# Performance work log

Hardware: AMD Instinct MI355X
Metric: run time of the kernel (lower is better)

## Reference

```python
import jax, jax.numpy as jnp
import numpy as np

N = 100000
E = 1600000
IN_DIM, HID, OUT = 128, 64, 64


def _gat(x, src, dst, W, a_src, a_dst, b, n):
    h = x @ W                                   # [N, F]
    a_s = (h * a_src).sum(-1)                   # [N]
    a_d = (h * a_dst).sum(-1)
    e = jax.nn.leaky_relu(a_s[src] + a_d[dst], negative_slope=0.2)  # [E]
    m = jax.ops.segment_max(e, dst, num_segments=n)
    ex = jnp.exp(e - m[dst])
    denom = jax.ops.segment_sum(ex, dst, num_segments=n)
    coef = ex / jnp.maximum(denom[dst], 1e-16)
    out = jax.ops.segment_sum(h[src] * coef[:, None], dst, num_segments=n)
    return out + b


def _gcn(x, src, dst, W, b, n):
    deg = jax.ops.segment_sum(jnp.ones_like(src, dtype=x.dtype), dst, num_segments=n)
    dinv = jnp.where(deg > 0, deg ** -0.5, 0.0)
    norm = dinv[src] * dinv[dst]                # [E]
    h = x @ W
    out = jax.ops.segment_sum(h[src] * norm[:, None], dst, num_segments=n)
    return out + b


def setup_inputs() -> dict:
    key = jax.random.key(0)
    ks = jax.random.split(key, 24)
    g = lambda k, shp, fan: jax.random.normal(k, shp, dtype=jnp.float32) * (1.0 / np.sqrt(fan))
    inp = {}
    inp['features'] = jax.random.normal(ks[0], (N, IN_DIM), dtype=jnp.float32)
    inp['edge_index'] = jax.random.randint(ks[1], (2, E), 0, N, dtype=jnp.int64)
    inp['node_mask'] = jax.random.randint(ks[2], (N,), 0, 2, dtype=jnp.int32)
    # GAT layer 1 (in->hid) and 2 (hid->out)
    inp['W_gat1'] = g(ks[3], (IN_DIM, HID), IN_DIM)
    inp['a_src1'] = g(ks[4], (HID,), HID)
    inp['a_dst1'] = g(ks[5], (HID,), HID)
    inp['b_gat1'] = jnp.zeros((HID,), jnp.float32)
    inp['W_gat2'] = g(ks[6], (HID, OUT), HID)
    inp['a_src2'] = g(ks[7], (OUT,), OUT)
    inp['a_dst2'] = g(ks[8], (OUT,), OUT)
    inp['b_gat2'] = jnp.zeros((OUT,), jnp.float32)
    # GCN layers
    inp['W_gcn1'] = g(ks[9], (IN_DIM, HID), IN_DIM)
    inp['b_gcn1'] = jnp.zeros((HID,), jnp.float32)
    inp['W_gcn2'] = g(ks[10], (HID, OUT), HID)
    inp['b_gcn2'] = jnp.zeros((OUT,), jnp.float32)
    # Decoder fc: 2*OUT -> IN_DIM
    inp['W_dec'] = g(ks[11], (2 * OUT, IN_DIM), 2 * OUT)
    inp['b_dec'] = jnp.zeros((IN_DIM,), jnp.float32)
    # Discriminator
    inp['W_d1'] = g(ks[12], (2 * OUT, 64), 2 * OUT)
    inp['b_d1'] = jnp.zeros((64,), jnp.float32)
    inp['W_d2'] = g(ks[13], (64, 32), 64)
    inp['b_d2'] = jnp.zeros((32,), jnp.float32)
    inp['W_d3'] = g(ks[14], (32, 1), 32)
    inp['b_d3'] = jnp.zeros((1,), jnp.float32)
    return inp


def reference(features, edge_index, node_mask,
              W_gat1, a_src1, a_dst1, b_gat1,
              W_gat2, a_src2, a_dst2, b_gat2,
              W_gcn1, b_gcn1, W_gcn2, b_gcn2,
              W_dec, b_dec,
              W_d1, b_d1, W_d2, b_d2, W_d3, b_d3):
    n = features.shape[0]
    src, dst = edge_index[0], edge_index[1]
    # node masking (eval-deterministic stand-in for mask_by_nodes_)
    x = jnp.where((node_mask == 1)[:, None], 0.0, features)
    # GAT branch (dropout is identity in eval mode)
    h_gat = jax.nn.elu(_gat(x, src, dst, W_gat1, a_src1, a_dst1, b_gat1, n))
    h_gat = _gat(h_gat, src, dst, W_gat2, a_src2, a_dst2, b_gat2, n)
    # GCN branch
    h_gcn = jax.nn.relu(_gcn(x, src, dst, W_gcn1, b_gcn1, n))
    h_gcn = _gcn(h_gcn, src, dst, W_gcn2, b_gcn2, n)
    encoded = jnp.concatenate([h_gat, h_gcn], axis=1)  # [N, 2*OUT]
    recon = jax.nn.relu(encoded @ W_dec + b_dec)        # Decoder (dropout off)
    d = jax.nn.relu(encoded @ W_d1 + b_d1)
    d = jax.nn.sigmoid(d @ W_d2 + b_d2)
    disc = d @ W_d3 + b_d3                              # [N, 1]
    return recon, encoded, disc
```

## Files before the change

kernel.cpp:

```cpp
#include <hip/hip_runtime.h>
#include <math.h>


#define INF_F __int_as_float(0x7f800000)
#define NSHARD 8

typedef __attribute__((ext_vector_type(8))) short bh8;
typedef __attribute__((ext_vector_type(4))) float f32x4;

__device__ __forceinline__ long edge_at(const void* p, int is64, long i) {
    if (is64) return (long)((const long long*)p)[i];
    return (long)((const int*)p)[i];
}

__device__ __forceinline__ unsigned short f2bf(float f) {
    unsigned u = __float_as_uint(f);
    return (unsigned short)((u + 0x7FFFu + ((u >> 16) & 1u)) >> 16);
}
__device__ __forceinline__ float bflo(unsigned p) { return __uint_as_float(p << 16); }
__device__ __forceinline__ float bfhi(unsigned p) { return __uint_as_float(p & 0xFFFF0000u); }
__device__ __forceinline__ unsigned pk2bf(float a, float b) {
    return (unsigned)f2bf(a) | ((unsigned)f2bf(b) << 16);
}

__global__ void k_detect(const int* ew, long words, int* flag) {
    long t = (long)blockIdx.x * blockDim.x + threadIdx.x;
    long stride = words / 8192; if (stride < 1) stride = 1;
    long w = 2 * (t * stride) + 1;
    if (t < 4096 && w < words) {
        if (ew[w] != 0) atomicOr(flag, 1);
    }
}

__global__ void k_deg(const void* edges, long E, const int* flag, int* deg) {
    long e = (long)blockIdx.x * blockDim.x + threadIdx.x;
    if (e >= E) return;
    int is64 = (*flag == 0);
    int d = (int)edge_at(edges, is64, E + e);
    atomicAdd(&deg[d], 1);
}

__global__ void k_scanA(const int* deg, int N, int* offs, int* blockSums) {
    __shared__ int s[256];
    int t = threadIdx.x;
    int i = blockIdx.x * 256 + t;
    int v = (i < N) ? deg[i] : 0;
    s[t] = v;
    for (int off = 1; off < 256; off <<= 1) {
        __syncthreads();
        int u = (t >= off) ? s[t - off] : 0;
        __syncthreads();
        s[t] += u;
    }
    __syncthreads();
    if (i < N) offs[i] = s[t] - v;
    if (t == 255) blockSums[blockIdx.x] = s[255];
}

__global__ void k_scanB(const int* blockSums, int nb, int* blockOff) {
    __shared__ int s[1024];
    int t = threadIdx.x;
    int v = (t < nb) ? blockSums[t] : 0;
    s[t] = v;
    for (int off = 1; off < 1024; off <<= 1) {
        __syncthreads();
        int u = (t >= off) ? s[t - off] : 0;
        __syncthreads();
        s[t] += u;
    }
    __syncthreads();
    if (t < nb) blockOff[t] = s[t] - v;
}

__global__ void k_scanC(int* offs, const int* blockOff, const int* deg,
                        float* dinv, int N, long E) {
    int i = blockIdx.x * 256 + threadIdx.x;
    if (i < N) {
        offs[i] += blockOff[i >> 8];
        int dg = deg[i];
        dinv[i] = dg > 0 ? rsqrtf((float)dg) : 0.0f;
    }
    if (i == 0) offs[N] = (int)E;
}

__global__ void k_fill(const void* edges, long E, const int* flag,
                       const int* offs, int* cursor, int* csr_src, int npp) {
    int bid = blockIdx.x;
    int shard = bid & (NSHARD - 1);
    long e = (long)(bid >> 3) * blockDim.x + threadIdx.x;
    if (e >= E) return;
    int is64 = (*flag == 0);
    int d = (int)edge_at(edges, is64, E + e);
    if (d / npp != shard) return;
    int s = (int)edge_at(edges, is64, e);
    int pos = offs[d] + atomicAdd(&cursor[d], 1);
    csr_src[pos] = s << 8;
}

__global__ __launch_bounds__(512) void k_dense1(
    const float* __restrict__ x, const int* __restrict__ mask,
    const float* __restrict__ Wa, const float* __restrict__ Wg,
    const float* __restrict__ aSrc, const float* __restrict__ aDst,
    const float* __restrict__ dinv,
    unsigned short* __restrict__ h16,
    float* __restrict__ a_s, float* __restrict__ a_d, int N)
{
    __shared__ float sW[8192 + 16 + 8192];
    int t = threadIdx.x;
    for (int i = t; i < 2048; i += 512) {
        ((float4*)sW)[i] = ((const float4*)Wa)[i];
        ((float4*)(sW + 8208))[i] = ((const float4*)Wg)[i];
    }
    __syncthreads();
    int base = blockIdx.x * 64;
    int tx = t & 31, ny = t >> 5;
    bool gat = tx < 16;
    int jc = (tx & 15) * 4;
    const float* Wp = gat ? sW : (sW + 8208);
    int gn0 = base + ny * 4;
    const float4* xp[4]; float mz[4];
#pragma unroll
    for (int n = 0; n < 4; ++n) {
        int gn = gn0 + n;
        int cl = (gn < N) ? gn : 0;
        xp[n] = (const float4*)(x + (long)cl * 128);
        mz[n] = (gn < N && mask[cl] != 1) ? 1.f : 0.f;
    }
    float acc[4][4];
#pragma unroll
    for (int n = 0; n < 4; ++n) { acc[n][0] = acc[n][1] = acc[n][2] = acc[n][3] = 0.f; }
#pragma unroll 2
    for (int k0 = 0; k0 < 128; k0 += 4) {
        float4 w[4];
#pragma unroll
        for (int kk = 0; kk < 4; ++kk) w[kk] = *(const float4*)&Wp[(k0 + kk) * 64 + jc];
        float4 xr[4];
#pragma unroll
        for (int n = 0; n < 4; ++n) xr[n] = xp[n][k0 >> 2];
#pragma unroll
        for (int kk = 0; kk < 4; ++kk) {
#pragma unroll
            for (int n = 0; n < 4; ++n) {
                float xv = (&xr[n].x)[kk];
                acc[n][0] = fmaf(xv, w[kk].x, acc[n][0]);
                acc[n][1] = fmaf(xv, w[kk].y, acc[n][1]);
                acc[n][2] = fmaf(xv, w[kk].z, acc[n][2]);
                acc[n][3] = fmaf(xv, w[kk].w, acc[n][3]);
            }
        }
    }
#pragma unroll
    for (int n = 0; n < 4; ++n) {
        acc[n][0] *= mz[n]; acc[n][1] *= mz[n]; acc[n][2] *= mz[n]; acc[n][3] *= mz[n];
    }
    float4 as4 = make_float4(0.f, 0.f, 0.f, 0.f), ad4 = as4;
    if (gat) { as4 = *(const float4*)&aSrc[jc]; ad4 = *(const float4*)&aDst[jc]; }
#pragma unroll
    for (int n = 0; n < 4; ++n) {
        int gn = gn0 + n;
        float pa = acc[n][0] * as4.x + acc[n][1] * as4.y + acc[n][2] * as4.z + acc[n][3] * as4.w;
        float pd = acc[n][0] * ad4.x + acc[n][1] * ad4.y + acc[n][2] * ad4.z + acc[n][3] * ad4.w;
#pragma unroll
        for (int off = 8; off; off >>= 1) { pa += __shfl_xor(pa, off); pd += __shfl_xor(pd, off); }
        if (gn < N) {
            if (gat) {
                if (tx == 0) { a_s[gn] = pa; a_d[gn] = pd; }
                ushort4 pk;
                pk.x = f2bf(acc[n][0]); pk.y = f2bf(acc[n][1]);
                pk.z = f2bf(acc[n][2]); pk.w = f2bf(acc[n][3]);
                *(ushort4*)&h16[(long)gn * 128 + jc] = pk;
            } else {
                float dv = dinv[gn];
                ushort4 pk;
                pk.x = f2bf(acc[n][0] * dv); pk.y = f2bf(acc[n][1] * dv);
                pk.z = f2bf(acc[n][2] * dv); pk.w = f2bf(acc[n][3] * dv);
                *(ushort4*)&h16[(long)gn * 128 + 64 + jc] = pk;
            }
        }
    }
}

__global__ __launch_bounds__(512) void k_dense2(
    const float* __restrict__ o,
    const float* __restrict__ Wa, const float* __restrict__ Wg,
    const float* __restrict__ aSrc, const float* __restrict__ aDst,
    const float* __restrict__ dinv,
    unsigned short* __restrict__ h16,
    float* __restrict__ a_s, float* __restrict__ a_d, int N)
{
    __shared__ float sW[4096 + 16 + 4096];
    int t = threadIdx.x;
    for (int i = t; i < 1024; i += 512) {
        ((float4*)sW)[i] = ((const float4*)Wa)[i];
        ((float4*)(sW + 4112))[i] = ((const float4*)Wg)[i];
    }
    __syncthreads();
    int base = blockIdx.x * 64;
    int tx = t & 31, ny = t >> 5;
    bool gat = tx < 16;
    int jc = (tx & 15) * 4;
    const float* Wp = gat ? sW : (sW + 4112);
    int xoff = gat ? 0 : 16;
    int gn0 = base + ny * 4;
    const float4* xp[4];
#pragma unroll
    for (int n = 0; n < 4; ++n) {
        int gn = gn0 + n;
        int cl = (gn < N) ? gn : 0;
        xp[n] = (const float4*)(o + (long)cl * 128) + xoff;
    }
    float acc[4][4];
#pragma unroll
    for (int n = 0; n < 4; ++n) { acc[n][0] = acc[n][1] = acc[n][2] = acc[n][3] = 0.f; }
#pragma unroll 2
    for (int k0 = 0; k0 < 64; k0 += 4) {
        float4 w[4];
#pragma unroll
        for (int kk = 0; kk < 4; ++kk) w[kk] = *(const float4*)&Wp[(k0 + kk) * 64 + jc];
        float4 xr[4];
#pragma unroll
        for (int n = 0; n < 4; ++n) xr[n] = xp[n][k0 >> 2];
#pragma unroll
        for (int kk = 0; kk < 4; ++kk) {
#pragma unroll
            for (int n = 0; n < 4; ++n) {
                float xv = (&xr[n].x)[kk];
                acc[n][0] = fmaf(xv, w[kk].x, acc[n][0]);
                acc[n][1] = fmaf(xv, w[kk].y, acc[n][1]);
                acc[n][2] = fmaf(xv, w[kk].z, acc[n][2]);
                acc[n][3] = fmaf(xv, w[kk].w, acc[n][3]);
            }
        }
    }
    float4 as4 = make_float4(0.f, 0.f, 0.f, 0.f), ad4 = as4;
    if (gat) { as4 = *(const float4*)&aSrc[jc]; ad4 = *(const float4*)&aDst[jc]; }
#pragma unroll
    for (int n = 0; n < 4; ++n) {
        int gn = gn0 + n;
        float pa = acc[n][0] * as4.x + acc[n][1] * as4.y + acc[n][2] * as4.z + acc[n][3] * as4.w;
        float pd = acc[n][0] * ad4.x + acc[n][1] * ad4.y + acc[n][2] * ad4.z + acc[n][3] * ad4.w;
#pragma unroll
        for (int off = 8; off; off >>= 1) { pa += __shfl_xor(pa, off); pd += __shfl_xor(pd, off); }
        if (gn < N) {
            if (gat) {
                if (tx == 0) { a_s[gn] = pa; a_d[gn] = pd; }
                ushort4 pk;
                pk.x = f2bf(acc[n][0]); pk.y = f2bf(acc[n][1]);
                pk.z = f2bf(acc[n][2]); pk.w = f2bf(acc[n][3]);
                *(ushort4*)&h16[(long)gn * 128 + jc] = pk;
            } else {
                float dv = dinv[gn];
                ushort4 pk;
                pk.x = f2bf(acc[n][0] * dv); pk.y = f2bf(acc[n][1] * dv);
                pk.z = f2bf(acc[n][2] * dv); pk.w = f2bf(acc[n][3] * dv);
                *(ushort4*)&h16[(long)gn * 128 + 64 + jc] = pk;
            }
        }
    }
}

template <int MODE>
__global__ __launch_bounds__(512) void k_agg(
    const int* __restrict__ offs, const int* __restrict__ csr,
    const float* __restrict__ a_s, const float* __restrict__ a_d,
    const float* __restrict__ dinv,
    const unsigned short* __restrict__ h16,
    const float* __restrict__ b_a, const float* __restrict__ b_g,
    float* __restrict__ out, unsigned* __restrict__ enc16, int N)
{
    int node = blockIdx.x * 8 + (threadIdx.x >> 6);
    int lane = threadIdx.x & 63;
    if (node >= N) return;
    int p0 = offs[node], p1 = offs[node + 1];
    int deg = p1 - p0;
    float adst = a_d[node];
    float dv = dinv[node];
    bool gat = lane < 32;
    const char* hb = (const char*)h16 + lane * 4;

    float2 res = make_float2(0.f, 0.f);
    if (deg > 0 && deg <= 64) {
        int soff = (lane < deg) ? csr[p0 + lane] : 0;
        float att = -INF_F;
        if (lane < deg) {
            float a = a_s[soff >> 8] + adst;
            att = a >= 0.f ? a : 0.2f * a;
        }
        float m = att;
#pragma unroll
        for (int off = 32; off; off >>= 1) m = fmaxf(m, __shfl_xor(m, off));
        float w = (lane < deg) ? __expf(att - m) : 0.f;
        float den = w;
#pragma unroll
        for (int off = 32; off; off >>= 1) den += __shfl_xor(den, off);
        float coef = w / den;

        float2 a0 = make_float2(0.f, 0.f), a1 = a0, a2 = a0, a3 = a0;
        int e = 0;
        for (; e + 4 <= deg; e += 4) {
            int o0 = __shfl(soff, e),     o1 = __shfl(soff, e + 1);
            int o2 = __shfl(soff, e + 2), o3 = __shfl(soff, e + 3);
            float c0 = __shfl(coef, e),     c1 = __shfl(coef, e + 1);
            float c2 = __shfl(coef, e + 2), c3 = __shfl(coef, e + 3);
            unsigned v0 = *(const unsigned*)(hb + o0);
            unsigned v1 = *(const unsigned*)(hb + o1);
            unsigned v2 = *(const unsigned*)(hb + o2);
            unsigned v3 = *(const unsigned*)(hb + o3);
            float w0 = gat ? c0 : 1.f, w1 = gat ? c1 : 1.f;
            float w2 = gat ? c2 : 1.f, w3 = gat ? c3 : 1.f;
            a0.x = fmaf(bflo(v0), w0, a0.x); a0.y = fmaf(bfhi(v0), w0, a0.y);
            a1.x = fmaf(bflo(v1), w1, a1.x); a1.y = fmaf(bfhi(v1), w1, a1.y);
            a2.x = fmaf(bflo(v2), w2, a2.x); a2.y = fmaf(bfhi(v2), w2, a2.y);
            a3.x = fmaf(bflo(v3), w3, a3.x); a3.y = fmaf(bfhi(v3), w3, a3.y);
        }
        for (; e < deg; ++e) {
            int oe = __shfl(soff, e);
            float ce = __shfl(coef, e);
            unsigned v = *(const unsigned*)(hb + oe);
            float we = gat ? ce : 1.f;
            a0.x = fmaf(bflo(v), we, a0.x); a0.y = fmaf(bfhi(v), we, a0.y);
        }
        res.x = (a0.x + a1.x) + (a2.x + a3.x);
        res.y = (a0.y + a1.y) + (a2.y + a3.y);
    } else if (deg > 64) {
        float m = -INF_F, den = 0.f;
        float2 aa = make_float2(0.f, 0.f);
        for (int p = p0; p < p1; ++p) {
            int soff = csr[p];
            float a = a_s[soff >> 8] + adst;
            float att = a >= 0.f ? a : 0.2f * a;
            float mn = fmaxf(m, att);
            float r = __expf(m - mn);
            float w = __expf(att - mn);
            den = den * r + w;
            unsigned v = *(const unsigned*)(hb + soff);
            float reff = gat ? r : 1.f, weff = gat ? w : 1.f;
            aa.x = fmaf(aa.x, reff, weff * bflo(v));
            aa.y = fmaf(aa.y, reff, weff * bfhi(v));
            m = mn;
        }
        if (gat) { res.x = aa.x / den; res.y = aa.y / den; }
        else     { res = aa; }
    }

    int col = lane * 2;
    float2 ov;
    if (gat) {
        ov.x = res.x + b_a[col];
        ov.y = res.y + b_a[col + 1];
        if (MODE == 0) {
            ov.x = ov.x > 0.f ? ov.x : (__expf(ov.x) - 1.f);
            ov.y = ov.y > 0.f ? ov.y : (__expf(ov.y) - 1.f);
        }
    } else {
        ov.x = dv * res.x + b_g[col - 64];
        ov.y = dv * res.y + b_g[col - 63];
        if (MODE == 0) {
            ov.x = fmaxf(ov.x, 0.f);
            ov.y = fmaxf(ov.y, 0.f);
        }
    }
    *(float2*)&out[(long)node * 128 + col] = ov;
    if (MODE == 1) enc16[(long)node * 64 + lane] = pk2bf(ov.x, ov.y);
}

__global__ __launch_bounds__(512) void k_dense3(
    const unsigned short* __restrict__ enc16,
    const float* __restrict__ Wdec, const float* __restrict__ bdec,
    const float* __restrict__ Wd1, const float* __restrict__ bd1,
    const float* __restrict__ Wd2, const float* __restrict__ bd2,
    const float* __restrict__ Wd3, const float* __restrict__ bd3,
    float* __restrict__ recon, float* __restrict__ disc, int N)
{
    __shared__ unsigned short sBdec[8 * 4 * 64 * 8];
    __shared__ unsigned short sBd1[4 * 4 * 64 * 8];
    __shared__ unsigned short sBd2[2 * 2 * 64 * 8];
    __shared__ unsigned short sd1[128 * 64];
    __shared__ float sWd3[32];
    int t = threadIdx.x;
    for (int slot = t; slot < 2048; slot += 512) {
        int l = slot & 63, ntks = slot >> 6, ks = ntks & 3, nt = ntks >> 2;
        int krow = ks * 32 + ((l >> 4) << 3);
        int col = nt * 16 + (l & 15);
#pragma unroll
        for (int j = 0; j < 8; ++j)
            sBdec[slot * 8 + j] = f2bf(Wdec[(krow + j) * 128 + col]);
    }
    for (int slot = t; slot < 1024; slot += 512) {
        int l = slot & 63, ntks = slot >> 6, ks = ntks & 3, nt = ntks >> 2;
        int krow = ks * 32 + ((l >> 4) << 3);
        int col = nt * 16 + (l & 15);
#pragma unroll
        for (int j = 0; j < 8; ++j)
            sBd1[slot * 8 + j] = f2bf(Wd1[(krow + j) * 64 + col]);
    }
    if (t < 256) {
        int slot = t;
        int l = slot & 63, ntks = slot >> 6, ks = ntks & 1, nt = ntks >> 1;
        int krow = ks * 32 + ((l >> 4) << 3);
        int col = nt * 16 + (l & 15);
#pragma unroll
        for (int j = 0; j < 8; ++j)
            sBd2[slot * 8 + j] = f2bf(Wd2[(krow + j) * 32 + col]);
    }
    if (t < 32) sWd3[t] = Wd3[t];
    __syncthreads();

    int w = t >> 6, lane = t & 63;
    int base = blockIdx.x * 128 + w * 16;
    int arow = base + (lane & 15);
    int acl = arow < N ? arow : 0;
    const unsigned short* ap = enc16 + (long)acl * 128 + ((lane >> 4) << 3);

    f32x4 accR[8], accD1[4];
#pragma unroll
    for (int i = 0; i < 8; ++i) accR[i] = (f32x4){0.f, 0.f, 0.f, 0.f};
#pragma unroll
    for (int i = 0; i < 4; ++i) accD1[i] = (f32x4){0.f, 0.f, 0.f, 0.f};
#pragma unroll
    for (int ks = 0; ks < 4; ++ks) {
        bh8 a = *(const bh8*)(ap + ks * 32);
#pragma unroll
        for (int nt = 0; nt < 8; ++nt) {
            bh8 b = *(const bh8*)&sBdec[((nt * 4 + ks) * 64 + lane) * 8];
            accR[nt] = __builtin_amdgcn_mfma_f32_16x16x32_bf16(a, b, accR[nt], 0, 0, 0);
        }
#pragma unroll
        for (int nt = 0; nt < 4; ++nt) {
            bh8 b = *(const bh8*)&sBd1[((nt * 4 + ks) * 64 + lane) * 8];
            accD1[nt] = __builtin_amdgcn_mfma_f32_16x16x32_bf16(a, b, accD1[nt], 0, 0, 0);
        }
    }
    int rb = base + ((lane >> 4) << 2);
#pragma unroll
    for (int nt = 0; nt < 8; ++nt) {
        int col = nt * 16 + (lane & 15);
        float bcol = bdec[col];
#pragma unroll
        for (int r = 0; r < 4; ++r) {
            int grow = rb + r;
            if (grow < N)
                recon[(long)grow * 128 + col] = fmaxf(accR[nt][r] + bcol, 0.f);
        }
    }
    int lrb = w * 16 + ((lane >> 4) << 2);
#pragma unroll
    for (int nt = 0; nt < 4; ++nt) {
        int col = nt * 16 + (lane & 15);
        float bcol = bd1[col];
#pragma unroll
        for (int r = 0; r < 4; ++r)
            sd1[(lrb + r) * 64 + col] = f2bf(fmaxf(accD1[nt][r] + bcol, 0.f));
    }
    __syncthreads();
    f32x4 accD2[2];
    accD2[0] = (f32x4){0.f, 0.f, 0.f, 0.f};
    accD2[1] = (f32x4){0.f, 0.f, 0.f, 0.f};
#pragma unroll
    for (int ks = 0; ks < 2; ++ks) {
        bh8 a = *(const bh8*)&sd1[(w * 16 + (lane & 15)) * 64 + ks * 32 + ((lane >> 4) << 3)];
#pragma unroll
        for (int nt = 0; nt < 2; ++nt) {
            bh8 b = *(const bh8*)&sBd2[((nt * 2 + ks) * 64 + lane) * 8];
            accD2[nt] = __builtin_amdgcn_mfma_f32_16x16x32_bf16(a, b, accD2[nt], 0, 0, 0);
        }
    }
    float b2a = bd2[lane & 15], b2b = bd2[16 + (lane & 15)];
    float w3a = sWd3[lane & 15], w3b = sWd3[16 + (lane & 15)];
    float b3 = bd3[0];
#pragma unroll
    for (int r = 0; r < 4; ++r) {
        float v = w3a / (1.f + __expf(-(accD2[0][r] + b2a)))
                + w3b / (1.f + __expf(-(accD2[1][r] + b2b)));
        v += __shfl_xor(v, 1); v += __shfl_xor(v, 2);
        v += __shfl_xor(v, 4); v += __shfl_xor(v, 8);
        int grow = rb + r;
        if ((lane & 15) == 0 && grow < N) disc[grow] = v + b3;
    }
}

extern "C" void kernel_launch(void* const* d_in, const int* in_sizes, int n_in,
                              void* d_out, int out_size, void* d_ws, size_t ws_size,
                              hipStream_t stream)
{
    const float* features = (const float*)d_in[0];
    const void*  edges    = d_in[1];
    const int*   mask     = (const int*)d_in[2];
    const float* W_gat1 = (const float*)d_in[3];
    const float* a_src1 = (const float*)d_in[4];
    const float* a_dst1 = (const float*)d_in[5];
    const float* b_gat1 = (const float*)d_in[6];
    const float* W_gat2 = (const float*)d_in[7];
    const float* a_src2 = (const float*)d_in[8];
    const float* a_dst2 = (const float*)d_in[9];
    const float* b_gat2 = (const float*)d_in[10];
    const float* W_gcn1 = (const float*)d_in[11];
    const float* b_gcn1 = (const float*)d_in[12];
    const float* W_gcn2 = (const float*)d_in[13];
    const float* b_gcn2 = (const float*)d_in[14];
    const float* W_dec  = (const float*)d_in[15];
    const float* b_dec  = (const float*)d_in[16];
    const float* W_d1   = (const float*)d_in[17];
    const float* b_d1   = (const float*)d_in[18];
    const float* W_d2   = (const float*)d_in[19];
    const float* b_d2   = (const float*)d_in[20];
    const float* W_d3   = (const float*)d_in[21];
    const float* b_d3   = (const float*)d_in[22];

    const int  N = in_sizes[0] / 128;
    const long E = (long)in_sizes[1] / 2;

    size_t nP = ((size_t)N + 255) & ~(size_t)255;
    size_t eP = ((size_t)E + 255) & ~(size_t)255;
    int*   deg       = (int*)d_ws;
    int*   offs      = deg + nP;
    int*   cursor    = offs + nP + 256;
    float* dinv      = (float*)(cursor + nP);
    float* a_s       = dinv + nP;
    float* a_d       = a_s + nP;
    int*   flag      = (int*)(a_d + nP);
    int*   blockSums = flag + 256;
    int*   blockOff  = blockSums + 1024;
    int*   csr       = blockOff + 1024;
    unsigned short* h16 = (unsigned short*)(csr + eP);
    float* o         = (float*)(h16 + nP * 128);
    unsigned* enc16  = (unsigned*)(o + nP * 128);

    hipMemsetAsync(deg, 0, nP * sizeof(int), stream);
    hipMemsetAsync(cursor, 0, nP * sizeof(int), stream);
    hipMemsetAsync(flag, 0, sizeof(int), stream);

    k_detect<<<16, 256, 0, stream>>>((const int*)edges, 2 * E, flag);

    unsigned eB = (unsigned)((E + 255) / 256);
    k_deg<<<eB, 256, 0, stream>>>(edges, E, flag, deg);

    int nbA = (N + 255) / 256;
    k_scanA<<<nbA, 256, 0, stream>>>(deg, N, offs, blockSums);
    k_scanB<<<1, 1024, 0, stream>>>(blockSums, nbA, blockOff);
    k_scanC<<<nbA, 256, 0, stream>>>(offs, blockOff, deg, dinv, N, E);
    int npp = (N + NSHARD - 1) / NSHARD;
    k_fill<<<eB * NSHARD, 256, 0, stream>>>(edges, E, flag, offs, cursor, csr, npp);

    unsigned dB = (unsigned)((N + 63) / 64);
    unsigned aB = (unsigned)((N + 7) / 8);
    unsigned mB = (unsigned)((N + 127) / 128);

    k_dense1<<<dB, 512, 0, stream>>>(features, mask, W_gat1, W_gcn1,
                                     a_src1, a_dst1, dinv,
                                     h16, a_s, a_d, N);
    k_agg<0><<<aB, 512, 0, stream>>>(offs, csr, a_s, a_d, dinv, h16,
                                     b_gat1, b_gcn1, o, nullptr, N);
    k_dense2<<<dB, 512, 0, stream>>>(o, W_gat2, W_gcn2,
                                     a_src2, a_dst2, dinv,
                                     h16, a_s, a_d, N);
    float* out = (float*)d_out;
    float* enc = out + (long)N * 128;
    k_agg<1><<<aB, 512, 0, stream>>>(offs, csr, a_s, a_d, dinv, h16,
                                     b_gat2, b_gcn2, enc, enc16, N);
    k_dense3<<<mB, 512, 0, stream>>>((const unsigned short*)enc16,
                                     W_dec, b_dec, W_d1, b_d1,
                                     W_d2, b_d2, W_d3, b_d3,
                                     out, out + (long)N * 256, N);
}
```

Before: 472.8 us.

## Use bf16 MFMA for layer-1/2 dense projections and store hidden activations as bf16

Replaces the two scalar-FMA fp32 dense kernels with a single templated kernel using 16x16x32 bf16 MFMA instructions. Weights are converted to bf16 fragments in shared memory, with a block-diagonal weight for layer 2. The first aggregation now writes its hidden output only as packed bf16 instead of fp32, halving that intermediate's write and read traffic. This adds bf16 rounding of inputs and weights before the matmul, and the h16 stores become scalar 2-byte writes.

After: 401.0 us. 15.2% less time.

```diff
diff --git a/kernel.cpp b/kernel.cpp
--- a/kernel.cpp
+++ b/kernel.cpp
@@ -97,163 +97,114 @@
     csr_src[pos] = s << 8;
 }
 
-__global__ __launch_bounds__(512) void k_dense1(
-    const float* __restrict__ x, const int* __restrict__ mask,
+template <int MODE>
+__global__ __launch_bounds__(512) void k_denseM(
+    const float* __restrict__ xf, const unsigned short* __restrict__ a16,
+    const int* __restrict__ mask,
     const float* __restrict__ Wa, const float* __restrict__ Wg,
     const float* __restrict__ aSrc, const float* __restrict__ aDst,
     const float* __restrict__ dinv,
     unsigned short* __restrict__ h16,
     float* __restrict__ a_s, float* __restrict__ a_d, int N)
 {
-    __shared__ float sW[8192 + 16 + 8192];
+    __shared__ unsigned short sB[8 * 4 * 64 * 8];
+    __shared__ float sAs[64], sAd[64];
     int t = threadIdx.x;
-    for (int i = t; i < 2048; i += 512) {
-        ((float4*)sW)[i] = ((const float4*)Wa)[i];
-        ((float4*)(sW + 8208))[i] = ((const float4*)Wg)[i];
-    }
+    for (int slot = t; slot < 2048; slot += 512) {
+        int l = slot & 63, ntks = slot >> 6, ks = ntks & 3, nt = ntks >> 2;
+        int col = nt * 16 + (l & 15);
+        int kbase = ks * 32 + ((l >> 4) << 3);
+#pragma unroll
+        for (int j = 0; j < 8; ++j) {
+            int k = kbase + j;
+            float v;
+            if (MODE == 0) {
+                v = (col < 64) ? Wa[k * 64 + col] : Wg[k * 64 + (col - 64)];
+            } else {
+                if (col < 64) v = (k < 64) ? Wa[k * 64 + col] : 0.f;
+                else          v = (k >= 64) ? Wg[(k - 64) * 64 + (col - 64)] : 0.f;
+            }
+            sB[slot * 8 + j] = f2bf(v);
+        }
+    }
+    if (t < 64) { sAs[t] = aSrc[t]; sAd[t] = aDst[t]; }
     __syncthreads();
-    int base = blockIdx.x * 64;
-    int tx = t & 31, ny = t >> 5;
-    bool gat = tx < 16;
-    int jc = (tx & 15) * 4;
-    const float* Wp = gat ? sW : (sW + 8208);
-    int gn0 = base + ny * 4;
-    const float4* xp[4]; float mz[4];
-#pragma unroll
-    for (int n = 0; n < 4; ++n) {
-        int gn = gn0 + n;
-        int cl = (gn < N) ? gn : 0;
-        xp[n] = (const float4*)(x + (long)cl * 128);
-        mz[n] = (gn < N && mask[cl] != 1) ? 1.f : 0.f;
-    }
-    float acc[4][4];
-#pragma unroll
-    for (int n = 0; n < 4; ++n) { acc[n][0] = acc[n][1] = acc[n][2] = acc[n][3] = 0.f; }
-#pragma unroll 2
-    for (int k0 = 0; k0 < 128; k0 += 4) {
-        float4 w[4];
-#pragma unroll
-        for (int kk = 0; kk < 4; ++kk) w[kk] = *(const float4*)&Wp[(k0 + kk) * 64 + jc];
-        float4 xr[4];
-#pragma unroll
-        for (int n = 0; n < 4; ++n) xr[n] = xp[n][k0 >> 2];
-#pragma unroll
-        for (int kk = 0; kk < 4; ++kk) {
-#pragma unroll
-            for (int n = 0; n < 4; ++n) {
-                float xv = (&xr[n].x)[kk];
-                acc[n][0] = fmaf(xv, w[kk].x, acc[n][0]);
-                acc[n][1] = fmaf(xv, w[kk].y, acc[n][1]);
-                acc[n][2] = fmaf(xv, w[kk].z, acc[n][2]);
-                acc[n][3] = fmaf(xv, w[kk].w, acc[n][3]);
-            }
-        }
-    }
-#pragma unroll
-    for (int n = 0; n < 4; ++n) {
-        acc[n][0] *= mz[n]; acc[n][1] *= mz[n]; acc[n][2] *= mz[n]; acc[n][3] *= mz[n];
-    }
-    float4 as4 = make_float4(0.f, 0.f, 0.f, 0.f), ad4 = as4;
-    if (gat) { as4 = *(const float4*)&aSrc[jc]; ad4 = *(const float4*)&aDst[jc]; }
-#pragma unroll
-    for (int n = 0; n < 4; ++n) {
-        int gn = gn0 + n;
-        float pa = acc[n][0] * as4.x + acc[n][1] * as4.y + acc[n][2] * as4.z + acc[n][3] * as4.w;
-        float pd = acc[n][0] * ad4.x + acc[n][1] * ad4.y + acc[n][2] * ad4.z + acc[n][3] * ad4.w;
-#pragma unroll
-        for (int off = 8; off; off >>= 1) { pa += __shfl_xor(pa, off); pd += __shfl_xor(pd, off); }
-        if (gn < N) {
-            if (gat) {
-                if (tx == 0) { a_s[gn] = pa; a_d[gn] = pd; }
-                ushort4 pk;
-                pk.x = f2bf(acc[n][0]); pk.y = f2bf(acc[n][1]);
-                pk.z = f2bf(acc[n][2]); pk.w = f2bf(acc[n][3]);
-                *(ushort4*)&h16[(long)gn * 128 + jc] = pk;
-            } else {
-                float dv = dinv[gn];
-                ushort4 pk;
-                pk.x = f2bf(acc[n][0] * dv); pk.y = f2bf(acc[n][1] * dv);
-                pk.z = f2bf(acc[n][2] * dv); pk.w = f2bf(acc[n][3] * dv);
-                *(ushort4*)&h16[(long)gn * 128 + 64 + jc] = pk;
-            }
-        }
-    }
-}
-
-__global__ __launch_bounds__(512) void k_dense2(
-    const float* __restrict__ o,
-    const float* __restrict__ Wa, const float* __restrict__ Wg,
-    const float* __restrict__ aSrc, const float* __restrict__ aDst,
-    const float* __restrict__ dinv,
-    unsigned short* __restrict__ h16,
-    float* __restrict__ a_s, float* __restrict__ a_d, int N)
-{
-    __shared__ float sW[4096 + 16 + 4096];
-    int t = threadIdx.x;
-    for (int i = t; i < 1024; i += 512) {
-        ((float4*)sW)[i] = ((const float4*)Wa)[i];
-        ((float4*)(sW + 4112))[i] = ((const float4*)Wg)[i];
-    }
-    __syncthreads();
-    int base = blockIdx.x * 64;
-    int tx = t & 31, ny = t >> 5;
-    bool gat = tx < 16;
-    int jc = (tx & 15) * 4;
-    const float* Wp = gat ? sW : (sW + 4112);
-    int xoff = gat ? 0 : 16;
-    int gn0 = base + ny * 4;
-    const float4* xp[4];
-#pragma unroll
-    for (int n = 0; n < 4; ++n) {
-        int gn = gn0 + n;
-        int cl = (gn < N) ? gn : 0;
-        xp[n] = (const float4*)(o + (long)cl * 128) + xoff;
-    }
-    float acc[4][4];
-#pragma unroll
-    for (int n = 0; n < 4; ++n) { acc[n][0] = acc[n][1] = acc[n][2] = acc[n][3] = 0.f; }
-#pragma unroll 2
-    for (int k0 = 0; k0 < 64; k0 += 4) {
-        float4 w[4];
-#pragma unroll
-        for (int kk = 0; kk < 4; ++kk) w[kk] = *(const float4*)&Wp[(k0 + kk) * 64 + jc];
-        float4 xr[4];
-#pragma unroll
-        for (int n = 0; n < 4; ++n) xr[n] = xp[n][k0 >> 2];
-#pragma unroll
-        for (int kk = 0; kk < 4; ++kk) {
-#pragma unroll
-            for (int n = 0; n < 4; ++n) {
-                float xv = (&xr[n].x)[kk];
-                acc[n][0] = fmaf(xv, w[kk].x, acc[n][0]);
-                acc[n][1] = fmaf(xv, w[kk].y, acc[n][1]);
-                acc[n][2] = fmaf(xv, w[kk].z, acc[n][2]);
-                acc[n][3] = fmaf(xv, w[kk].w, acc[n][3]);
-            }
-        }
-    }
-    float4 as4 = make_float4(0.f, 0.f, 0.f, 0.f), ad4 = as4;
-    if (gat) { as4 = *(const float4*)&aSrc[jc]; ad4 = *(const float4*)&aDst[jc]; }
-#pragma unroll
-    for (int n = 0; n < 4; ++n) {
-        int gn = gn0 + n;
-        float pa = acc[n][0] * as4.x + acc[n][1] * as4.y + acc[n][2] * as4.z + acc[n][3] * as4.w;
-        float pd = acc[n][0] * ad4.x + acc[n][1] * ad4.y + acc[n][2] * ad4.z + acc[n][3] * ad4.w;
-#pragma unroll
-        for (int off = 8; off; off >>= 1) { pa += __shfl_xor(pa, off); pd += __shfl_xor(pd, off); }
-        if (gn < N) {
-            if (gat) {
-                if (tx == 0) { a_s[gn] = pa; a_d[gn] = pd; }
-                ushort4 pk;
-                pk.x = f2bf(acc[n][0]); pk.y = f2bf(acc[n][1]);
-                pk.z = f2bf(acc[n][2]); pk.w = f2bf(acc[n][3]);
-                *(ushort4*)&h16[(long)gn * 128 + jc] = pk;
-            } else {
-                float dv = dinv[gn];
-                ushort4 pk;
-                pk.x = f2bf(acc[n][0] * dv); pk.y = f2bf(acc[n][1] * dv);
-                pk.z = f2bf(acc[n][2] * dv); pk.w = f2bf(acc[n][3] * dv);
-                *(ushort4*)&h16[(long)gn * 128 + 64 + jc] = pk;
+
+    int w = t >> 6, lane = t & 63;
+    int base = blockIdx.x * 128 + w * 16;
+    int arow = base + (lane & 15);
+    int acl = arow < N ? arow : 0;
+
+    bh8 afr[4];
+    if (MODE == 0) {
+        float msk = (arow < N && mask[acl] != 1) ? 1.f : 0.f;
+        const float* ap = xf + (long)acl * 128 + ((lane >> 4) << 3);
+#pragma unroll
+        for (int ks = 0; ks < 4; ++ks) {
+            float4 u0 = *(const float4*)(ap + ks * 32);
+            float4 u1 = *(const float4*)(ap + ks * 32 + 4);
+            union { bh8 v; unsigned u4[4]; } cv;
+            cv.u4[0] = pk2bf(u0.x * msk, u0.y * msk);
+            cv.u4[1] = pk2bf(u0.z * msk, u0.w * msk);
+            cv.u4[2] = pk2bf(u1.x * msk, u1.y * msk);
+            cv.u4[3] = pk2bf(u1.z * msk, u1.w * msk);
+            afr[ks] = cv.v;
+        }
+    } else {
+        const unsigned short* ap = a16 + (long)acl * 128 + ((lane >> 4) << 3);
+#pragma unroll
+        for (int ks = 0; ks < 4; ++ks) afr[ks] = *(const bh8*)(ap + ks * 32);
+    }
+
+    f32x4 acc[8];
+#pragma unroll
+    for (int i = 0; i < 8; ++i) acc[i] = (f32x4){0.f, 0.f, 0.f, 0.f};
+#pragma unroll
+    for (int ks = 0; ks < 4; ++ks) {
+#pragma unroll
+        for (int nt = 0; nt < 8; ++nt) {
+            bh8 b = *(const bh8*)&sB[((nt * 4 + ks) * 64 + lane) * 8];
+            acc[nt] = __builtin_amdgcn_mfma_f32_16x16x32_bf16(afr[ks], b, acc[nt], 0, 0, 0);
+        }
+    }
+
+    int rb = base + ((lane >> 4) << 2);
+    float dvr[4];
+#pragma unroll
+    for (int r = 0; r < 4; ++r) dvr[r] = (rb + r < N) ? dinv[rb + r] : 0.f;
+
+    float pa[4] = {0.f, 0.f, 0.f, 0.f}, pd[4] = {0.f, 0.f, 0.f, 0.f};
+#pragma unroll
+    for (int nt = 0; nt < 4; ++nt) {
+        float as = sAs[nt * 16 + (lane & 15)];
+        float ad = sAd[nt * 16 + (lane & 15)];
+#pragma unroll
+        for (int r = 0; r < 4; ++r) {
+            pa[r] = fmaf(acc[nt][r], as, pa[r]);
+            pd[r] = fmaf(acc[nt][r], ad, pd[r]);
+        }
+    }
+#pragma unroll
+    for (int r = 0; r < 4; ++r) {
+#pragma unroll
+        for (int off = 8; off; off >>= 1) {
+            pa[r] += __shfl_xor(pa[r], off);
+            pd[r] += __shfl_xor(pd[r], off);
+        }
+        int grow = rb + r;
+        if ((lane & 15) == 0 && grow < N) { a_s[grow] = pa[r]; a_d[grow] = pd[r]; }
+    }
+#pragma unroll
+    for (int nt = 0; nt < 8; ++nt) {
+        int col = nt * 16 + (lane & 15);
+        bool gcn = nt >= 4;
+#pragma unroll
+        for (int r = 0; r < 4; ++r) {
+            int grow = rb + r;
+            if (grow < N) {
+                float v = acc[nt][r];
+                if (gcn) v *= dvr[r];
+                h16[(long)grow * 128 + col] = f2bf(v);
             }
         }
     }
@@ -266,7 +217,7 @@
     const float* __restrict__ dinv,
     const unsigned short* __restrict__ h16,
     const float* __restrict__ b_a, const float* __restrict__ b_g,
-    float* __restrict__ out, unsigned* __restrict__ enc16, int N)
+    float* __restrict__ out, unsigned* __restrict__ o16, int N)
 {
     int node = blockIdx.x * 8 + (threadIdx.x >> 6);
     int lane = threadIdx.x & 63;
@@ -360,8 +311,8 @@
             ov.y = fmaxf(ov.y, 0.f);
         }
     }
-    *(float2*)&out[(long)node * 128 + col] = ov;
-    if (MODE == 1) enc16[(long)node * 64 + lane] = pk2bf(ov.x, ov.y);
+    if (MODE == 1) *(float2*)&out[(long)node * 128 + col] = ov;
+    o16[(long)node * 64 + lane] = pk2bf(ov.x, ov.y);
 }
 
 __global__ __launch_bounds__(512) void k_dense3(
@@ -523,8 +474,8 @@
     int*   blockOff  = blockSums + 1024;
     int*   csr       = blockOff + 1024;
     unsigned short* h16 = (unsigned short*)(csr + eP);
-    float* o         = (float*)(h16 + nP * 128);
-    unsigned* enc16  = (unsigned*)(o + nP * 128);
+    unsigned* o16    = (unsigned*)(h16 + nP * 128);
+    unsigned* enc16  = o16 + nP * 64;
 
     hipMemsetAsync(deg, 0, nP * sizeof(int), stream);
     hipMemsetAsync(cursor, 0, nP * sizeof(int), stream);
@@ -542,18 +493,17 @@
     int npp = (N + NSHARD - 1) / NSHARD;
     k_fill<<<eB * NSHARD, 256, 0, stream>>>(edges, E, flag, offs, cursor, csr, npp);
 
-    unsigned dB = (unsigned)((N + 63) / 64);
     unsigned aB = (unsigned)((N + 7) / 8);
     unsigned mB = (unsigned)((N + 127) / 128);
 
-    k_dense1<<<dB, 512, 0, stream>>>(features, mask, W_gat1, W_gcn1,
-                                     a_src1, a_dst1, dinv,
-                                     h16, a_s, a_d, N);
+    k_denseM<0><<<mB, 512, 0, stream>>>(features, nullptr, mask,
+                                        W_gat1, W_gcn1, a_src1, a_dst1, dinv,
+                                        h16, a_s, a_d, N);
     k_agg<0><<<aB, 512, 0, stream>>>(offs, csr, a_s, a_d, dinv, h16,
-                                     b_gat1, b_gcn1, o, nullptr, N);
-    k_dense2<<<dB, 512, 0, stream>>>(o, W_gat2, W_gcn2,
-                                     a_src2, a_dst2, dinv,
-                                     h16, a_s, a_d, N);
+                                     b_gat1, b_gcn1, nullptr, o16, N);
+    k_denseM<1><<<mB, 512, 0, stream>>>(nullptr, (const unsigned short*)o16, nullptr,
+                                        W_gat2, W_gcn2, a_src2, a_dst2, dinv,
+                                        h16, a_s, a_d, N);
     float* out = (float*)d_out;
     float* enc = out + (long)N * 128;
     k_agg<1><<<aB, 512, 0, stream>>>(offs, csr, a_s, a_d, dinv, h16,
```
